# Kernel optimization log

Measured on AMD Instinct MI355X. Metric: run time of the kernel, lower is better.

The kernel has to match this reference:

```python
import jax, jax.numpy as jnp
import numpy as np

B, T, C, H = 4, 1024, 512, 8
HD = C // H
N_NODE, F_DIM, TOTAL_DIM = 64, 8, 16
SCALE = 1.0 / np.sqrt(HD)


def _build_mask():
    # causal tril with every (total_dim-1 mod total_dim)-th COLUMN zeroed
    m = np.tril(np.ones((T, T), dtype=np.float32))
    m[:, TOTAL_DIM - 1::TOTAL_DIM] = 0.0
    return jnp.asarray(m)

MASK = _build_mask()  # (T, T), 1 = keep, 0 = mask


def setup_inputs() -> dict:
    key = jax.random.key(0)
    ks = jax.random.split(key, 12)
    s = 0.02
    return {
        "x": jax.random.normal(ks[0], (B, T, C), dtype=jnp.float32),
        "attn_bias": jax.random.normal(ks[1], (H, N_NODE, N_NODE), dtype=jnp.float32) * 0.1,
        "Wq": jax.random.normal(ks[2], (C, C), dtype=jnp.float32) * s,
        "bq": jax.random.normal(ks[3], (C,), dtype=jnp.float32) * s,
        "Wk": jax.random.normal(ks[4], (C, C), dtype=jnp.float32) * s,
        "bk": jax.random.normal(ks[5], (C,), dtype=jnp.float32) * s,
        "Wv": jax.random.normal(ks[6], (C, C), dtype=jnp.float32) * s,
        "bv": jax.random.normal(ks[7], (C,), dtype=jnp.float32) * s,
        "Wp": jax.random.normal(ks[8], (C, C), dtype=jnp.float32) * s,
        "bp": jax.random.normal(ks[9], (C,), dtype=jnp.float32) * s,
    }


def reference(x, attn_bias, Wq, bq, Wk, bk, Wv, bv, Wp, bp):
    Bx, Tx, Cx = x.shape

    def heads(W, b):  # (B,T,C) -> (B,H,T,HD); torch Linear is x @ W.T + b
        return (x @ W.T + b).reshape(Bx, Tx, H, HD).transpose(0, 2, 1, 3)

    q, k, v = heads(Wq, bq), heads(Wk, bk), heads(Wv, bv)

    # repeat_interleave + repeat expansion == kron(attn_bias, ones(f_dim, f_dim))
    d = N_NODE * F_DIM
    bias = jnp.repeat(jnp.repeat(attn_bias, F_DIM, axis=1), F_DIM, axis=2)  # (H, d, d)
    padded_bias = jnp.zeros((H, Tx, Tx), dtype=x.dtype).at[:, :d, :d].set(bias)

    att = jnp.einsum('bhqd,bhkd->bhqk', q, k) * SCALE + padded_bias[None]
    neg = jnp.asarray(-jnp.inf, dtype=att.dtype)
    att = jnp.where(MASK[None, None, :Tx, :Tx] == 0, neg, att)
    att = jax.nn.softmax(att, axis=-1)

    y = jnp.einsum('bhqk,bhkd->bhqd', att, v)
    y = y.transpose(0, 2, 1, 3).reshape(Bx, Tx, Cx)
    return y @ Wp.T + bp
```

## Files before the change

kernel.cpp:

```cpp
#include <hip/hip_runtime.h>

#define T_SEQ 1024
#define C_DIM 512
#define H_HEADS 8
#define HDIM 64
#define B_BATCH 4
#define M_ROWS (B_BATCH * T_SEQ)

typedef __attribute__((ext_vector_type(8))) short short8;
typedef __attribute__((ext_vector_type(4))) float f32x4;

__device__ __forceinline__ unsigned short f2bf(float f) {
    unsigned u = __builtin_bit_cast(unsigned, f);
    u += 0x7FFFu + ((u >> 16) & 1u);
    return (unsigned short)(u >> 16);
}

__global__ __launch_bounds__(256) void cast_all(
    const float* __restrict__ x,
    const float* __restrict__ wq, const float* __restrict__ wk,
    const float* __restrict__ wv, const float* __restrict__ wp,
    unsigned short* __restrict__ xb,
    unsigned short* __restrict__ wqb, unsigned short* __restrict__ wkb,
    unsigned short* __restrict__ wvb, unsigned short* __restrict__ wpb)
{
    const long NX = (long)M_ROWS * C_DIM;
    const long NW = (long)C_DIM * C_DIM;
    long i4 = (long)blockIdx.x * blockDim.x + threadIdx.x;
    long base = i4 * 4;
    const float* src; unsigned short* dst; long off;
    if (base < NX) { src = x; dst = xb; off = base; }
    else {
        long r = base - NX;
        int w = (int)(r >> 18);
        off = r & (NW - 1);
        switch (w) {
            case 0:  src = wq; dst = wqb; break;
            case 1:  src = wk; dst = wkb; break;
            case 2:  src = wv; dst = wvb; break;
            default: src = wp; dst = wpb; break;
        }
    }
    float4 v = *(const float4*)(src + off);
    ushort4 o;
    o.x = f2bf(v.x); o.y = f2bf(v.y); o.z = f2bf(v.z); o.w = f2bf(v.w);
    *(ushort4*)(dst + off) = o;
}

template <bool BHTD>
__device__ __forceinline__ void gemm_body(
    const unsigned short* __restrict__ A,
    const unsigned short* __restrict__ W,
    const float* __restrict__ bias,
    unsigned short* __restrict__ Obf,
    float* __restrict__ Of)
{
    __shared__ __align__(16) unsigned short Al[64 * 72];
    __shared__ __align__(16) unsigned short Bl[64 * 72];

    const int tid  = threadIdx.x;
    const int w    = tid >> 6;
    const int lane = tid & 63;
    const int quad = lane >> 4;
    const int l16  = lane & 15;
    const int m0   = blockIdx.x * 64;
    const int n0   = blockIdx.y * 64;

    f32x4 acc[4] = {};

    for (int k0 = 0; k0 < 512; k0 += 64) {
        __syncthreads();
        for (int it = 0; it < 2; ++it) {
            int ch = tid + 256 * it;
            int r = ch >> 3, c8 = ch & 7;
            *(short8*)&Al[r * 72 + c8 * 8] =
                *(const short8*)&A[(long)(m0 + r) * 512 + k0 + c8 * 8];
            *(short8*)&Bl[r * 72 + c8 * 8] =
                *(const short8*)&W[(long)(n0 + r) * 512 + k0 + c8 * 8];
        }
        __syncthreads();
        for (int s = 0; s < 2; ++s) {
            short8 af = *(const short8*)&Al[(16 * w + l16) * 72 + 32 * s + 8 * quad];
            for (int ct = 0; ct < 4; ++ct) {
                short8 bf = *(const short8*)&Bl[(16 * ct + l16) * 72 + 32 * s + 8 * quad];
                acc[ct] = __builtin_amdgcn_mfma_f32_16x16x32_bf16(af, bf, acc[ct], 0, 0, 0);
            }
        }
    }

    for (int ct = 0; ct < 4; ++ct) {
        int col = n0 + 16 * ct + l16;
        float bv = bias[col];
        for (int reg = 0; reg < 4; ++reg) {
            int row = m0 + 16 * w + 4 * quad + reg;
            float v = acc[ct][reg] + bv;
            if (BHTD) {
                int b = row >> 10, t = row & 1023;
                int h = col >> 6,  hd = col & 63;
                Obf[(((long)(b * H_HEADS + h)) * T_SEQ + t) * HDIM + hd] = f2bf(v);
            } else {
                Of[(long)row * 512 + col] = v;
            }
        }
    }
}

__global__ __launch_bounds__(256) void gemm_qkv(
    const unsigned short* __restrict__ A,
    const unsigned short* __restrict__ Wq, const unsigned short* __restrict__ Wk,
    const unsigned short* __restrict__ Wv,
    const float* __restrict__ bq, const float* __restrict__ bk, const float* __restrict__ bv,
    unsigned short* __restrict__ Q, unsigned short* __restrict__ K,
    unsigned short* __restrict__ V)
{
    const unsigned short* W; const float* b; unsigned short* O;
    if (blockIdx.z == 0)      { W = Wq; b = bq; O = Q; }
    else if (blockIdx.z == 1) { W = Wk; b = bk; O = K; }
    else                      { W = Wv; b = bv; O = V; }
    gemm_body<true>(A, W, b, O, nullptr);
}

__global__ __launch_bounds__(256) void gemm_out_k(
    const unsigned short* __restrict__ A, const unsigned short* __restrict__ W,
    const float* __restrict__ bias, float* __restrict__ O)
{
    gemm_body<false>(A, W, bias, nullptr, O);
}

__global__ __launch_bounds__(256) void attn(
    const unsigned short* __restrict__ Q, const unsigned short* __restrict__ K,
    const unsigned short* __restrict__ V, const float* __restrict__ attn_bias,
    unsigned short* __restrict__ Y)
{
    __shared__ __align__(16) unsigned short Kl[64 * 72];
    __shared__ __align__(16) unsigned short Vt[64 * 72];
    __shared__ __align__(16) unsigned short Pl[4][16 * 72];
    __shared__ float biasl[8][64];

    const int tid  = threadIdx.x;
    const int w    = tid >> 6;
    const int lane = tid & 63;
    const int quad = lane >> 4;
    const int l16  = lane & 15;
    const int bx   = blockIdx.x;
    const int bh   = blockIdx.y;
    const int h    = bh & 7;
    const int q0   = bx * 64;

    if (q0 < 512) {
        for (int i = tid; i < 512; i += 256) {
            int nq = (q0 >> 3) + (i >> 6);
            biasl[i >> 6][i & 63] = attn_bias[h * 4096 + nq * 64 + (i & 63)];
        }
    }

    const unsigned short* Qbh = Q + (long)bh * T_SEQ * HDIM;
    const unsigned short* Kbh = K + (long)bh * T_SEQ * HDIM;
    const unsigned short* Vbh = V + (long)bh * T_SEQ * HDIM;

    short8 qf[2];
    {
        int qr = q0 + 16 * w + l16;
        qf[0] = *(const short8*)&Qbh[(long)qr * HDIM + 8 * quad];
        qf[1] = *(const short8*)&Qbh[(long)qr * HDIM + 32 + 8 * quad];
    }

    f32x4 oacc[4] = {};
    float mrow[4] = {-INFINITY, -INFINITY, -INFINITY, -INFINITY};
    float lrow[4] = {0.f, 0.f, 0.f, 0.f};

    const int ntiles = bx + 1;
    for (int kt = 0; kt < ntiles; ++kt) {
        const int k0 = kt * 64;
        __syncthreads();
        for (int it = 0; it < 2; ++it) {
            int ch = tid + 256 * it;
            int r = ch >> 3, c8 = ch & 7;
            *(short8*)&Kl[r * 72 + c8 * 8] =
                *(const short8*)&Kbh[(long)(k0 + r) * HDIM + c8 * 8];
        }
        for (int it = 0; it < 2; ++it) {
            int ch = tid + 256 * it;
            int r = ch & 63, c8 = ch >> 6;
            short8 v = *(const short8*)&Vbh[(long)(k0 + r) * HDIM + c8 * 8];
            for (int j = 0; j < 8; ++j)
                Vt[(c8 * 8 + j) * 72 + r] = (unsigned short)v[j];
        }
        __syncthreads();

        f32x4 s[4] = {};
        for (int st = 0; st < 2; ++st) {
            for (int ct = 0; ct < 4; ++ct) {
                short8 bf = *(const short8*)&Kl[(16 * ct + l16) * 72 + 32 * st + 8 * quad];
                s[ct] = __builtin_amdgcn_mfma_f32_16x16x32_bf16(qf[st], bf, s[ct], 0, 0, 0);
            }
        }

        const int qrb = q0 + 16 * w + 4 * quad;
        float rmax[4] = {-INFINITY, -INFINITY, -INFINITY, -INFINITY};
        for (int ct = 0; ct < 4; ++ct) {
            int kcol = k0 + 16 * ct + l16;
            for (int reg = 0; reg < 4; ++reg) {
                int qrow = qrb + reg;
                float v = s[ct][reg] * 0.125f;
                if (qrow < 512 && kcol < 512)
                    v += biasl[(qrow >> 3) & 7][kcol >> 3];
                bool keep = (kcol <= qrow) && ((kcol & 15) != 15);
                v = keep ? v : -INFINITY;
                s[ct][reg] = v;
                rmax[reg] = fmaxf(rmax[reg], v);
            }
        }
        for (int off = 1; off < 16; off <<= 1)
            for (int reg = 0; reg < 4; ++reg)
                rmax[reg] = fmaxf(rmax[reg], __shfl_xor(rmax[reg], off));

        float alpha[4];
        for (int reg = 0; reg < 4; ++reg) {
            float mnew = fmaxf(mrow[reg], rmax[reg]);
            alpha[reg] = __expf(mrow[reg] - mnew);
            mrow[reg] = mnew;
        }

        float rsum[4] = {0.f, 0.f, 0.f, 0.f};
        for (int ct = 0; ct < 4; ++ct) {
            for (int reg = 0; reg < 4; ++reg) {
                float p = __expf(s[ct][reg] - mrow[reg]);
                rsum[reg] += p;
                Pl[w][(4 * quad + reg) * 72 + 16 * ct + l16] = f2bf(p);
            }
        }
        for (int off = 1; off < 16; off <<= 1)
            for (int reg = 0; reg < 4; ++reg)
                rsum[reg] += __shfl_xor(rsum[reg], off);
        for (int reg = 0; reg < 4; ++reg)
            lrow[reg] = lrow[reg] * alpha[reg] + rsum[reg];
        for (int ct = 0; ct < 4; ++ct)
            for (int reg = 0; reg < 4; ++reg)
                oacc[ct][reg] *= alpha[reg];

        for (int st = 0; st < 2; ++st) {
            short8 af = *(const short8*)&Pl[w][l16 * 72 + 32 * st + 8 * quad];
            for (int ct = 0; ct < 4; ++ct) {
                short8 bf = *(const short8*)&Vt[(16 * ct + l16) * 72 + 32 * st + 8 * quad];
                oacc[ct] = __builtin_amdgcn_mfma_f32_16x16x32_bf16(af, bf, oacc[ct], 0, 0, 0);
            }
        }
    }

    const int b = bh >> 3;
    for (int ct = 0; ct < 4; ++ct) {
        int hd = 16 * ct + l16;
        for (int reg = 0; reg < 4; ++reg) {
            int qrow = q0 + 16 * w + 4 * quad + reg;
            float o = oacc[ct][reg] / lrow[reg];
            Y[((long)b * T_SEQ + qrow) * C_DIM + h * HDIM + hd] = f2bf(o);
        }
    }
}

extern "C" void kernel_launch(void* const* d_in, const int* in_sizes, int n_in,
                              void* d_out, int out_size, void* d_ws, size_t ws_size,
                              hipStream_t stream)
{
    const float* x         = (const float*)d_in[0];
    const float* attn_bias = (const float*)d_in[1];
    const float* Wq = (const float*)d_in[2]; const float* bq = (const float*)d_in[3];
    const float* Wk = (const float*)d_in[4]; const float* bk = (const float*)d_in[5];
    const float* Wv = (const float*)d_in[6]; const float* bv = (const float*)d_in[7];
    const float* Wp = (const float*)d_in[8]; const float* bp = (const float*)d_in[9];
    float* out = (float*)d_out;

    const long NX = (long)M_ROWS * C_DIM;
    const long NW = (long)C_DIM * C_DIM;

    unsigned short* xb  = (unsigned short*)d_ws;
    unsigned short* wqb = xb  + NX;
    unsigned short* wkb = wqb + NW;
    unsigned short* wvb = wkb + NW;
    unsigned short* wpb = wvb + NW;
    unsigned short* Qb  = wpb + NW;
    unsigned short* Kb  = Qb  + NX;
    unsigned short* Vb  = Kb  + NX;
    unsigned short* Yb  = Vb  + NX;

    long n4 = (NX + 4 * NW) / 4;
    cast_all<<<dim3((unsigned)(n4 / 256)), 256, 0, stream>>>(
        x, Wq, Wk, Wv, Wp, xb, wqb, wkb, wvb, wpb);

    gemm_qkv<<<dim3(M_ROWS / 64, C_DIM / 64, 3), 256, 0, stream>>>(
        xb, wqb, wkb, wvb, bq, bk, bv, Qb, Kb, Vb);

    attn<<<dim3(T_SEQ / 64, B_BATCH * H_HEADS), 256, 0, stream>>>(
        Qb, Kb, Vb, attn_bias, Yb);

    gemm_out_k<<<dim3(M_ROWS / 64, C_DIM / 64), 256, 0, stream>>>(
        Yb, wpb, bp, out);
}
```

Measured before the change: 148.0 us.

## Split causal attention across KV chunks and pre-transpose V in QKV GEMM

Attention is now split-KV: each query tile's causal key range is cut into chunks of up to four 64-key tiles, giving 40 work items per head instead of 16 unevenly sized ones. Each item writes unnormalized partial outputs plus row max and sum to workspace, and a new combine kernel merges them. The QKV GEMM also writes V already transposed, so the attention kernel no longer scatters V into shared memory element by element. The cost is an extra kernel launch and fp32 partial-output traffic through global memory, plus strided scattered stores of V in the GEMM epilogue.

After: 142.6 us. 1.04x faster.

```diff
diff --git a/kernel.cpp b/kernel.cpp
--- a/kernel.cpp
+++ b/kernel.cpp
@@ -6,6 +6,7 @@
 #define HDIM 64
 #define B_BATCH 4
 #define M_ROWS (B_BATCH * T_SEQ)
+#define NSPLIT_TOT 40
 
 typedef __attribute__((ext_vector_type(8))) short short8;
 typedef __attribute__((ext_vector_type(4))) float f32x4;
@@ -15,6 +16,15 @@
     u += 0x7FFFu + ((u >> 16) & 1u);
     return (unsigned short)(u >> 16);
 }
+
+__device__ __constant__ unsigned char BX_OF[NSPLIT_TOT] =
+    {0,1,2,3,4,4,5,5,6,6,7,7,8,8,8,9,9,9,10,10,10,11,11,11,
+     12,12,12,12,13,13,13,13,14,14,14,14,15,15,15,15};
+__device__ __constant__ unsigned char SP_OF[NSPLIT_TOT] =
+    {0,0,0,0,0,1,0,1,0,1,0,1,0,1,2,0,1,2,0,1,2,0,1,2,
+     0,1,2,3,0,1,2,3,0,1,2,3,0,1,2,3};
+__device__ __constant__ unsigned char CUM_OF[16] =
+    {0,1,2,3,4,6,8,10,12,15,18,21,24,28,32,36};
 
 __global__ __launch_bounds__(256) void cast_all(
     const float* __restrict__ x,
@@ -47,13 +57,13 @@
     *(ushort4*)(dst + off) = o;
 }
 
-template <bool BHTD>
 __device__ __forceinline__ void gemm_body(
     const unsigned short* __restrict__ A,
     const unsigned short* __restrict__ W,
     const float* __restrict__ bias,
     unsigned short* __restrict__ Obf,
-    float* __restrict__ Of)
+    float* __restrict__ Of,
+    int mode)
 {
     __shared__ __align__(16) unsigned short Al[64 * 72];
     __shared__ __align__(16) unsigned short Bl[64 * 72];
@@ -94,12 +104,15 @@
         for (int reg = 0; reg < 4; ++reg) {
             int row = m0 + 16 * w + 4 * quad + reg;
             float v = acc[ct][reg] + bv;
-            if (BHTD) {
+            if (mode == 2) {
+                Of[(long)row * 512 + col] = v;
+            } else {
                 int b = row >> 10, t = row & 1023;
                 int h = col >> 6,  hd = col & 63;
-                Obf[(((long)(b * H_HEADS + h)) * T_SEQ + t) * HDIM + hd] = f2bf(v);
-            } else {
-                Of[(long)row * 512 + col] = v;
+                long idx = (mode == 0)
+                    ? ((((long)(b * H_HEADS + h)) * T_SEQ + t) * HDIM + hd)
+                    : ((((long)(b * H_HEADS + h)) * HDIM + hd) * T_SEQ + t);
+                Obf[idx] = f2bf(v);
             }
         }
     }
@@ -113,27 +126,27 @@
     unsigned short* __restrict__ Q, unsigned short* __restrict__ K,
     unsigned short* __restrict__ V)
 {
-    const unsigned short* W; const float* b; unsigned short* O;
-    if (blockIdx.z == 0)      { W = Wq; b = bq; O = Q; }
-    else if (blockIdx.z == 1) { W = Wk; b = bk; O = K; }
-    else                      { W = Wv; b = bv; O = V; }
-    gemm_body<true>(A, W, b, O, nullptr);
+    const unsigned short* W; const float* b; unsigned short* O; int mode;
+    if (blockIdx.z == 0)      { W = Wq; b = bq; O = Q; mode = 0; }
+    else if (blockIdx.z == 1) { W = Wk; b = bk; O = K; mode = 0; }
+    else                      { W = Wv; b = bv; O = V; mode = 1; }
+    gemm_body(A, W, b, O, nullptr, mode);
 }
 
 __global__ __launch_bounds__(256) void gemm_out_k(
     const unsigned short* __restrict__ A, const unsigned short* __restrict__ W,
     const float* __restrict__ bias, float* __restrict__ O)
 {
-    gemm_body<false>(A, W, bias, nullptr, O);
-}
-
-__global__ __launch_bounds__(256) void attn(
+    gemm_body(A, W, bias, nullptr, O, 2);
+}
+
+__global__ __launch_bounds__(256) void attn_split(
     const unsigned short* __restrict__ Q, const unsigned short* __restrict__ K,
-    const unsigned short* __restrict__ V, const float* __restrict__ attn_bias,
-    unsigned short* __restrict__ Y)
+    const unsigned short* __restrict__ Vt, const float* __restrict__ attn_bias,
+    float* __restrict__ Opart, float* __restrict__ mpart, float* __restrict__ lpart)
 {
     __shared__ __align__(16) unsigned short Kl[64 * 72];
-    __shared__ __align__(16) unsigned short Vt[64 * 72];
+    __shared__ __align__(16) unsigned short Vl[64 * 72];
     __shared__ __align__(16) unsigned short Pl[4][16 * 72];
     __shared__ float biasl[8][64];
 
@@ -142,21 +155,25 @@
     const int lane = tid & 63;
     const int quad = lane >> 4;
     const int l16  = lane & 15;
-    const int bx   = blockIdx.x;
+    const int sidx = blockIdx.x;
     const int bh   = blockIdx.y;
     const int h    = bh & 7;
+    const int bx   = BX_OF[sidx];
+    const int sp   = SP_OF[sidx];
     const int q0   = bx * 64;
-
-    if (q0 < 512) {
+    const int kt0  = sp * 4;
+    const int kt1  = min(kt0 + 4, bx + 1);
+
+    if (q0 < 512 && sp < 2) {
         for (int i = tid; i < 512; i += 256) {
             int nq = (q0 >> 3) + (i >> 6);
             biasl[i >> 6][i & 63] = attn_bias[h * 4096 + nq * 64 + (i & 63)];
         }
     }
 
-    const unsigned short* Qbh = Q + (long)bh * T_SEQ * HDIM;
-    const unsigned short* Kbh = K + (long)bh * T_SEQ * HDIM;
-    const unsigned short* Vbh = V + (long)bh * T_SEQ * HDIM;
+    const unsigned short* Qbh = Q  + (long)bh * T_SEQ * HDIM;
+    const unsigned short* Kbh = K  + (long)bh * T_SEQ * HDIM;
+    const unsigned short* Vbh = Vt + (long)bh * HDIM * T_SEQ;
 
     short8 qf[2];
     {
@@ -169,8 +186,7 @@
     float mrow[4] = {-INFINITY, -INFINITY, -INFINITY, -INFINITY};
     float lrow[4] = {0.f, 0.f, 0.f, 0.f};
 
-    const int ntiles = bx + 1;
-    for (int kt = 0; kt < ntiles; ++kt) {
+    for (int kt = kt0; kt < kt1; ++kt) {
         const int k0 = kt * 64;
         __syncthreads();
         for (int it = 0; it < 2; ++it) {
@@ -178,13 +194,8 @@
             int r = ch >> 3, c8 = ch & 7;
             *(short8*)&Kl[r * 72 + c8 * 8] =
                 *(const short8*)&Kbh[(long)(k0 + r) * HDIM + c8 * 8];
-        }
-        for (int it = 0; it < 2; ++it) {
-            int ch = tid + 256 * it;
-            int r = ch & 63, c8 = ch >> 6;
-            short8 v = *(const short8*)&Vbh[(long)(k0 + r) * HDIM + c8 * 8];
-            for (int j = 0; j < 8; ++j)
-                Vt[(c8 * 8 + j) * 72 + r] = (unsigned short)v[j];
+            *(short8*)&Vl[r * 72 + c8 * 8] =
+                *(const short8*)&Vbh[(long)r * T_SEQ + k0 + c8 * 8];
         }
         __syncthreads();
 
@@ -242,20 +253,66 @@
         for (int st = 0; st < 2; ++st) {
             short8 af = *(const short8*)&Pl[w][l16 * 72 + 32 * st + 8 * quad];
             for (int ct = 0; ct < 4; ++ct) {
-                short8 bf = *(const short8*)&Vt[(16 * ct + l16) * 72 + 32 * st + 8 * quad];
+                short8 bf = *(const short8*)&Vl[(16 * ct + l16) * 72 + 32 * st + 8 * quad];
                 oacc[ct] = __builtin_amdgcn_mfma_f32_16x16x32_bf16(af, bf, oacc[ct], 0, 0, 0);
             }
         }
     }
 
-    const int b = bh >> 3;
-    for (int ct = 0; ct < 4; ++ct) {
-        int hd = 16 * ct + l16;
+    const long p = (long)bh * NSPLIT_TOT + sidx;
+    float* Op = Opart + p * 4096;
+    for (int ct = 0; ct < 4; ++ct)
+        for (int reg = 0; reg < 4; ++reg)
+            Op[(16 * w + 4 * quad + reg) * 64 + 16 * ct + l16] = oacc[ct][reg];
+    if (l16 == 0) {
         for (int reg = 0; reg < 4; ++reg) {
-            int qrow = q0 + 16 * w + 4 * quad + reg;
-            float o = oacc[ct][reg] / lrow[reg];
-            Y[((long)b * T_SEQ + qrow) * C_DIM + h * HDIM + hd] = f2bf(o);
-        }
+            int qr = 16 * w + 4 * quad + reg;
+            mpart[p * 64 + qr] = mrow[reg];
+            lpart[p * 64 + qr] = lrow[reg];
+        }
+    }
+}
+
+__global__ __launch_bounds__(256) void attn_combine(
+    const float* __restrict__ Opart, const float* __restrict__ mpart,
+    const float* __restrict__ lpart, unsigned short* __restrict__ Y)
+{
+    const int bx = blockIdx.x, bh = blockIdx.y;
+    const int b = bh >> 3, h = bh & 7;
+    const int ns = (bx >> 2) + 1;
+    const long p0 = (long)bh * NSPLIT_TOT + CUM_OF[bx];
+    const int tid = threadIdx.x;
+    const int qr = tid >> 2;
+    const int hs = (tid & 3) * 16;
+
+    float m[4], l[4];
+    for (int s = 0; s < ns; ++s) {
+        m[s] = mpart[(p0 + s) * 64 + qr];
+        l[s] = lpart[(p0 + s) * 64 + qr];
+    }
+    float ms = -INFINITY;
+    for (int s = 0; s < ns; ++s) ms = fmaxf(ms, m[s]);
+    float L = 0.f, sc[4];
+    for (int s = 0; s < ns; ++s) { sc[s] = __expf(m[s] - ms); L += l[s] * sc[s]; }
+
+    float acc[16] = {};
+    for (int s = 0; s < ns; ++s) {
+        const float4* op = (const float4*)(Opart + (p0 + s) * 4096 + qr * 64 + hs);
+        float f = sc[s];
+        for (int j4 = 0; j4 < 4; ++j4) {
+            float4 v = op[j4];
+            acc[4 * j4 + 0] += f * v.x; acc[4 * j4 + 1] += f * v.y;
+            acc[4 * j4 + 2] += f * v.z; acc[4 * j4 + 3] += f * v.w;
+        }
+    }
+    float inv = 1.f / L;
+    int q = bx * 64 + qr;
+    unsigned short* y = Y + ((long)b * T_SEQ + q) * C_DIM + h * HDIM + hs;
+    for (int j4 = 0; j4 < 4; ++j4) {
+        ushort4 o;
+        o.x = f2bf(acc[4 * j4 + 0] * inv); o.y = f2bf(acc[4 * j4 + 1] * inv);
+        o.z = f2bf(acc[4 * j4 + 2] * inv); o.w = f2bf(acc[4 * j4 + 3] * inv);
+        *(ushort4*)(y + 4 * j4) = o;
     }
 }
 
@@ -281,18 +338,24 @@
     unsigned short* wpb = wvb + NW;
     unsigned short* Qb  = wpb + NW;
     unsigned short* Kb  = Qb  + NX;
-    unsigned short* Vb  = Kb  + NX;
-    unsigned short* Yb  = Vb  + NX;
+    unsigned short* Vtb = Kb  + NX;
+    unsigned short* Yb  = Vtb + NX;
+    float* Opart = (float*)(Yb + NX);
+    float* mpart = Opart + (long)32 * NSPLIT_TOT * 4096;
+    float* lpart = mpart + (long)32 * NSPLIT_TOT * 64;
 
     long n4 = (NX + 4 * NW) / 4;
     cast_all<<<dim3((unsigned)(n4 / 256)), 256, 0, stream>>>(
         x, Wq, Wk, Wv, Wp, xb, wqb, wkb, wvb, wpb);
 
     gemm_qkv<<<dim3(M_ROWS / 64, C_DIM / 64, 3), 256, 0, stream>>>(
-        xb, wqb, wkb, wvb, bq, bk, bv, Qb, Kb, Vb);
-
-    attn<<<dim3(T_SEQ / 64, B_BATCH * H_HEADS), 256, 0, stream>>>(
-        Qb, Kb, Vb, attn_bias, Yb);
+        xb, wqb, wkb, wvb, bq, bk, bv, Qb, Kb, Vtb);
+
+    attn_split<<<dim3(NSPLIT_TOT, B_BATCH * H_HEADS), 256, 0, stream>>>(
+        Qb, Kb, Vtb, attn_bias, Opart, mpart, lpart);
+
+    attn_combine<<<dim3(T_SEQ / 64, B_BATCH * H_HEADS), 256, 0, stream>>>(
+        Opart, mpart, lpart, Yb);
 
     gemm_out_k<<<dim3(M_ROWS / 64, C_DIM / 64), 256, 0, stream>>>(
         Yb, wpb, bp, out);
```
